# Optimization experiments

Hardware: AMD Instinct MI355X
Metric: run time of the kernel (lower is better)

## Reference

```python
import jax, jax.numpy as jnp
import numpy as np

B, L, D, F = 1, 4096, 4096, 11008
# (start, end, side): side 0 = vision expert, side 1 = language expert.
# Mirrors merge_section_size over alternating contiguous vision/language token ranges.
SEGMENTS = [(0, 1024, 0), (1024, 2048, 1), (2048, 3072, 0), (3072, 4096, 1)]


def setup_inputs() -> dict:
    key = jax.random.key(0)
    ks = jax.random.split(key, 7)
    s = 0.02  # weight init scale
    hidden_states = jax.random.normal(ks[0], (B, L, D), jnp.float32)
    tt = np.zeros((B, L), np.int32)
    for a, b, side in SEGMENTS:
        tt[:, a:b] = side
    token_type_ids = jnp.asarray(tt)
    lg_w = jax.random.normal(ks[1], (D, F), jnp.float32) * s
    lu_w = jax.random.normal(ks[2], (D, F), jnp.float32) * s
    ld_w = jax.random.normal(ks[3], (F, D), jnp.float32) * s
    vg_w = jax.random.normal(ks[4], (D, F), jnp.float32) * s
    vu_w = jax.random.normal(ks[5], (D, F), jnp.float32) * s
    vd_w = jax.random.normal(ks[6], (F, D), jnp.float32) * s
    return {
        'hidden_states': hidden_states,
        'token_type_ids': token_type_ids,
        'lg_w': lg_w, 'lu_w': lu_w, 'ld_w': ld_w,
        'vg_w': vg_w, 'vu_w': vu_w, 'vd_w': vd_w,
    }


def _swiglu_mlp(x, gw, uw, dw):
    # x: [B, T, D] -> [B, T, D]; down(silu(gate(x)) * up(x))
    h = jax.nn.silu(jnp.einsum('btd,df->btf', x, gw)) * jnp.einsum('btd,df->btf', x, uw)
    return jnp.einsum('btf,fd->btd', h, dw)


def reference(hidden_states, token_type_ids, lg_w, lu_w, ld_w, vg_w, vu_w, vd_w):
    # Split-dispatch over static contiguous segments, then concat along seq dim.
    outs = []
    for a, b, side in SEGMENTS:
        seg = hidden_states[:, a:b, :]
        if side == 1:
            outs.append(_swiglu_mlp(seg, lg_w, lu_w, ld_w))
        else:
            outs.append(_swiglu_mlp(seg, vg_w, vu_w, vd_w))
    return jnp.concatenate(outs, axis=1)
```

## Files before the change

### kernel.cpp

```cpp
#include <hip/hip_runtime.h>
#include <math.h>

typedef unsigned short u16;
typedef short s16x8 __attribute__((ext_vector_type(8)));
typedef float f32x4 __attribute__((ext_vector_type(4)));
typedef float f32x16 __attribute__((ext_vector_type(16)));

#define GLOAD16(gp, lp)                                                        \
  __builtin_amdgcn_global_load_lds(                                            \
      (const __attribute__((address_space(1))) void*)(gp),                     \
      (__attribute__((address_space(3))) void*)(lp), 16, 0, 0)

__device__ __forceinline__ u16 f2bf(float f) {
  union { float f; unsigned u; } v; v.f = f;
  unsigned r = v.u + 0x7fffu + ((v.u >> 16) & 1u);
  return (u16)(r >> 16);
}

__global__ __launch_bounds__(256) void cvt_x_kernel(const float* __restrict__ in,
                                                    u16* __restrict__ out) {
  size_t i = ((size_t)blockIdx.x * 256 + threadIdx.x) * 8;
  float4 a = *(const float4*)(in + i);
  float4 b = *(const float4*)(in + i + 4);
  s16x8 v;
  v[0] = (short)f2bf(a.x); v[1] = (short)f2bf(a.y);
  v[2] = (short)f2bf(a.z); v[3] = (short)f2bf(a.w);
  v[4] = (short)f2bf(b.x); v[5] = (short)f2bf(b.y);
  v[6] = (short)f2bf(b.z); v[7] = (short)f2bf(b.w);
  *(s16x8*)(out + i) = v;
}

__global__ __launch_bounds__(256) void transpose_cvt_kernel(
    const float* __restrict__ in0, const float* __restrict__ in1,
    const float* __restrict__ in2, const float* __restrict__ in3,
    const float* __restrict__ in4, const float* __restrict__ in5,
    u16* __restrict__ o01, u16* __restrict__ o23,
    u16* __restrict__ o4, u16* __restrict__ o5) {
  __shared__ float s[64 * 65];
  const int mat = blockIdx.y;
  const float* in; u16* out;
  switch (mat) {
    case 0: in = in0; out = o01; break;
    case 1: in = in1; out = o01; break;
    case 2: in = in2; out = o23; break;
    case 3: in = in3; out = o23; break;
    case 4: in = in4; out = o4; break;
    default: in = in5; out = o5; break;
  }
  const int R = (mat < 4) ? 4096 : 11008;
  const int C = (mat < 4) ? 11008 : 4096;
  const int nTc = C >> 6;
  const int tr = blockIdx.x / nTc, tc = blockIdx.x - tr * nTc;
  const int r0 = tr << 6, c0 = tc << 6;
  const int t = threadIdx.x;
#pragma unroll
  for (int p = 0; p < 4; ++p) {
    const int lr = p * 16 + (t >> 4);
    const int lc = (t & 15) * 4;
    float4 v = *(const float4*)(in + (size_t)(r0 + lr) * C + (c0 + lc));
    float* sp = &s[lr * 65 + lc];
    sp[0] = v.x; sp[1] = v.y; sp[2] = v.z; sp[3] = v.w;
  }
  __syncthreads();
#pragma unroll
  for (int q = 0; q < 2; ++q) {
    const int oc = q * 32 + (t >> 3);
    const int orr = (t & 7) * 8;
    s16x8 v;
#pragma unroll
    for (int i = 0; i < 8; ++i) v[i] = (short)f2bf(s[(orr + i) * 65 + oc]);
    const int f = c0 + oc;
    size_t orow;
    if (mat < 4) orow = (size_t)((f >> 7) << 8) + ((mat & 1) << 7) + (f & 127);
    else         orow = (size_t)f;
    *(s16x8*)(out + orow * R + (r0 + orr)) = v;
  }
}

#define SBAR() __builtin_amdgcn_s_barrier()
#define LGKM0() asm volatile("s_waitcnt lgkmcnt(0)")
#define VMCNT4() asm volatile("s_waitcnt vmcnt(4)")
#define VMCNT2() asm volatile("s_waitcnt vmcnt(2)")
#define VMCNT0() asm volatile("s_waitcnt vmcnt(0)")

#define LDA(d, mh)                                                             \
  do {                                                                         \
    _Pragma("unroll") for (int fj = 0; fj < 2; ++fj)                           \
        _Pragma("unroll") for (int ks = 0; ks < 4; ++ks)                       \
        af[fj][ks] = *(const s16x8*)(ldsA + (d) * 32768 + (mh) * 16384 +       \
                                     arow + fj * 4096 + cx[ks]);               \
  } while (0)
#define LDB(d, nh)                                                             \
  do {                                                                         \
    _Pragma("unroll") for (int ks = 0; ks < 4; ++ks)                           \
        bf[nh][ks] = *(const s16x8*)(ldsB + (d) * 32768 + (nh) * 16384 +       \
                                     brow + cx[ks]);                           \
  } while (0)
#define MFMA8(mh, nh)                                                          \
  do {                                                                         \
    __builtin_amdgcn_s_setprio(1);                                             \
    _Pragma("unroll") for (int fj = 0; fj < 2; ++fj)                           \
        _Pragma("unroll") for (int ks = 0; ks < 4; ++ks)                       \
        acc[mh][fj][nh] = __builtin_amdgcn_mfma_f32_32x32x16_bf16(             \
            af[fj][ks], bf[nh][ks], acc[mh][fj][nh], 0, 0, 0);                 \
    __builtin_amdgcn_s_setprio(0);                                             \
  } while (0)

#define STG_A(d, h, kt)                                                        \
  do {                                                                         \
    GLOAD16(srcA + (size_t)((h) * 128) * KB + (size_t)(kt) * 128,              \
            ldsA + (d) * 32768 + (h) * 16384 + woff);                          \
    GLOAD16(srcA + (size_t)((h) * 128 + 64) * KB + (size_t)(kt) * 128,         \
            ldsA + (d) * 32768 + (h) * 16384 + 8192 + woff);                   \
  } while (0)
#define STG_B(d, h, kt)                                                        \
  do {                                                                         \
    GLOAD16(srcB + (size_t)((h) * 128) * KB + (size_t)(kt) * 128,              \
            ldsB + (d) * 32768 + (h) * 16384 + woff);                          \
    GLOAD16(srcB + (size_t)((h) * 128 + 64) * KB + (size_t)(kt) * 128,         \
            ldsB + (d) * 32768 + (h) * 16384 + 8192 + woff);                   \
  } while (0)

__global__ __launch_bounds__(512, 1) void gemm_gateup_persist(
    const u16* __restrict__ A, const u16* __restrict__ GUl,
    const u16* __restrict__ GUv, const int* __restrict__ tt,
    u16* __restrict__ H, int* __restrict__ qcnt) {
  constexpr int KB = 8192;
  constexpr int NKT = 64;
  __shared__ u16 sA[2][2][128][64];
  __shared__ u16 sB[2][2][128][64];
  __shared__ int sQ;

  const int t = threadIdx.x;
  const int lane = t & 63;
  const int l31 = lane & 31;
  const int kg = lane >> 5;
  const int wn = (t >> 6) & 3;
  const int wm = (t >> 8) & 1;

  const int rowq = t >> 3;
  const int gsw = ((t & 7) ^ (rowq & 7)) << 4;
  char* ldsA = (char*)&sA[0][0][0][0];
  char* ldsB = (char*)&sB[0][0][0][0];
  const int woff = (t & 448) << 4;

  const int arow = (wm * 64 + l31) * 128;
  const int brow = (wn * 32 + l31) * 128;
  int cx[4];
#pragma unroll
  for (int ks = 0; ks < 4; ++ks) cx[ks] = ((2 * ks + kg) ^ (lane & 7)) << 4;

  for (;;) {
    __syncthreads();
    if (t == 0) sQ = atomicAdd(qcnt, 1);
    __syncthreads();
    const int q = sQ;
    if (q >= 1376) break;
    const int nT = q >> 4;
    const int mT = q & 15;
    const int side = tt[mT << 8];
    const u16* GU = side ? GUl : GUv;
    const char* srcA = (const char*)A + (size_t)(mT * 256 + rowq) * KB + gsw;
    const char* srcB = (const char*)GU + (size_t)(nT * 256 + rowq) * KB + gsw;

    s16x8 af[2][4], bf[2][4];
    f32x16 acc[2][2][2];
#pragma unroll
    for (int a = 0; a < 2; ++a)
#pragma unroll
      for (int b = 0; b < 2; ++b)
#pragma unroll
        for (int c = 0; c < 2; ++c)
#pragma unroll
          for (int r = 0; r < 16; ++r) acc[a][b][c][r] = 0.f;

    STG_A(0, 0, 0); STG_B(0, 0, 0); STG_B(0, 1, 0); STG_A(0, 1, 0);
    VMCNT4();
    SBAR();

    for (int T = 0; T < NKT - 1; ++T) {
      const int d = T & 1, nd = d ^ 1;
      LDA(d, 0); LDB(d, 0);
      STG_A(nd, 0, T + 1);
      LGKM0(); MFMA8(0, 0);
      VMCNT4(); SBAR();
      LDB(d, 1);
      STG_B(nd, 0, T + 1);
      LGKM0(); MFMA8(0, 1);
      VMCNT4(); SBAR();
      LDA(d, 1);
      STG_B(nd, 1, T + 1);
      LGKM0(); MFMA8(1, 1);
      STG_A(nd, 1, T + 1);
      MFMA8(1, 0);
      VMCNT4(); SBAR();
    }
    {
      const int d = (NKT - 1) & 1;
      LDA(d, 0); LDB(d, 0);
      LGKM0(); MFMA8(0, 0);
      VMCNT2(); SBAR();
      LDB(d, 1);
      LGKM0(); MFMA8(0, 1);
      VMCNT0(); SBAR();
      LDA(d, 1);
      LGKM0(); MFMA8(1, 1);
      MFMA8(1, 0);
    }

    const int f = nT * 128 + wn * 32 + l31;
#pragma unroll
    for (int mh = 0; mh < 2; ++mh)
#pragma unroll
      for (int fj = 0; fj < 2; ++fj) {
        const int rowbase = mT * 256 + mh * 128 + wm * 64 + fj * 32 + 4 * kg;
#pragma unroll
        for (int r = 0; r < 16; ++r) {
          const int row = rowbase + (r & 3) + 8 * (r >> 2);
          const float gv = acc[mh][fj][0][r];
          const float uv = acc[mh][fj][1][r];
          const float hv = gv / (1.f + __expf(-gv)) * uv;
          H[(size_t)row * 11008 + f] = f2bf(hv);
        }
      }
  }
}

__global__ __launch_bounds__(512, 1) void gemm_down(
    const u16* __restrict__ Hm, const u16* __restrict__ Dl,
    const u16* __restrict__ Dv, const int* __restrict__ tt,
    float* __restrict__ O) {
  constexpr int KB = 22016;
  constexpr int NKT = 172;
  __shared__ u16 sA[2][2][128][64];
  __shared__ u16 sB[2][2][128][64];

  const int bid = blockIdx.x;
  const int wg = (bid & 7) * 32 + (bid >> 3);
  const int mT = wg & 15;
  const int nT = wg >> 4;

  const int t = threadIdx.x;
  const int lane = t & 63;
  const int l31 = lane & 31;
  const int kg = lane >> 5;
  const int wn = (t >> 6) & 3;
  const int wm = (t >> 8) & 1;

  const int side = tt[mT << 8];
  const u16* B = side ? Dl : Dv;

  const int rowq = t >> 3;
  const int gsw = ((t & 7) ^ (rowq & 7)) << 4;
  const char* srcA = (const char*)Hm + (size_t)(mT * 256 + rowq) * KB + gsw;
  const char* srcB = (const char*)B + (size_t)(nT * 256 + rowq) * KB + gsw;
  char* ldsA = (char*)&sA[0][0][0][0];
  char* ldsB = (char*)&sB[0][0][0][0];
  const int woff = (t & 448) << 4;

  const int arow = (wm * 64 + l31) * 128;
  const int brow = (wn * 32 + l31) * 128;
  int cx[4];
#pragma unroll
  for (int ks = 0; ks < 4; ++ks) cx[ks] = ((2 * ks + kg) ^ (lane & 7)) << 4;

  s16x8 af[2][4], bf[2][4];
  f32x16 acc[2][2][2];
#pragma unroll
  for (int a = 0; a < 2; ++a)
#pragma unroll
    for (int b = 0; b < 2; ++b)
#pragma unroll
      for (int c = 0; c < 2; ++c)
#pragma unroll
        for (int r = 0; r < 16; ++r) acc[a][b][c][r] = 0.f;

  STG_A(0, 0, 0); STG_B(0, 0, 0); STG_B(0, 1, 0); STG_A(0, 1, 0);
  VMCNT4();
  SBAR();

  for (int T = 0; T < NKT - 1; ++T) {
    const int d = T & 1, nd = d ^ 1;
    LDA(d, 0); LDB(d, 0);
    STG_A(nd, 0, T + 1);
    LGKM0(); MFMA8(0, 0);
    VMCNT4(); SBAR();
    LDB(d, 1);
    STG_B(nd, 0, T + 1);
    LGKM0(); MFMA8(0, 1);
    VMCNT4(); SBAR();
    LDA(d, 1);
    STG_B(nd, 1, T + 1);
    LGKM0(); MFMA8(1, 1);
    STG_A(nd, 1, T + 1);
    MFMA8(1, 0);
    VMCNT4(); SBAR();
  }
  {
    const int d = (NKT - 1) & 1;
    LDA(d, 0); LDB(d, 0);
    LGKM0(); MFMA8(0, 0);
    VMCNT2(); SBAR();
    LDB(d, 1);
    LGKM0(); MFMA8(0, 1);
    VMCNT0(); SBAR();
    LDA(d, 1);
    LGKM0(); MFMA8(1, 1);
    MFMA8(1, 0);
  }

#pragma unroll
  for (int mh = 0; mh < 2; ++mh)
#pragma unroll
    for (int fj = 0; fj < 2; ++fj) {
      const int rowbase = mT * 256 + mh * 128 + wm * 64 + fj * 32 + 4 * kg;
#pragma unroll
      for (int nh = 0; nh < 2; ++nh) {
        const int col = nT * 256 + nh * 128 + wn * 32 + l31;
#pragma unroll
        for (int r = 0; r < 16; ++r) {
          const int row = rowbase + (r & 3) + 8 * (r >> 2);
          O[(size_t)row * 4096 + col] = acc[mh][fj][nh][r];
        }
      }
    }
}

extern "C" void kernel_launch(void* const* d_in, const int* in_sizes, int n_in,
                              void* d_out, int out_size, void* d_ws, size_t ws_size,
                              hipStream_t stream) {
  (void)in_sizes; (void)n_in; (void)out_size; (void)ws_size;
  const float* x  = (const float*)d_in[0];
  const int*   tt = (const int*)d_in[1];
  const float* lg = (const float*)d_in[2];
  const float* lu = (const float*)d_in[3];
  const float* ld = (const float*)d_in[4];
  const float* vg = (const float*)d_in[5];
  const float* vu = (const float*)d_in[6];
  const float* vd = (const float*)d_in[7];

  u16* ws  = (u16*)d_ws;
  u16* xbf = ws;
  u16* GUl = xbf + 16777216;
  u16* GUv = GUl + 90177536;
  u16* ldT = GUv + 90177536;
  u16* vdT = ldT + 45088768;
  u16* hbuf = vdT + 45088768;
  int* qcnt = (int*)(hbuf + 45088768);

  hipMemsetAsync(qcnt, 0, 4, stream);
  cvt_x_kernel<<<dim3(8192), dim3(256), 0, stream>>>(x, xbf);
  transpose_cvt_kernel<<<dim3(11008, 6), dim3(256), 0, stream>>>(
      lg, lu, vg, vu, ld, vd, GUl, GUv, ldT, vdT);
  gemm_gateup_persist<<<dim3(256), dim3(512), 0, stream>>>(
      xbf, GUl, GUv, tt, hbuf, qcnt);
  gemm_down<<<dim3(256), dim3(512), 0, stream>>>(hbuf, ldT, vdT, tt, (float*)d_out);
}
```

Baseline: 1.410 ms.

## Restructure GEMM main loop into 8-wave ping-pong pipeline with deeper prefetch

Replaces the per-k-tile main loop in both GEMMs with a shared macro that unrolls two k-tiles, issues loads for up to two tiles ahead, and wraps each MFMA cluster in barriers so wave groups alternate between loading and computing. Wait counts change to allow more global loads in flight. The LDS swizzle also gains an extra XOR term on row bits 3-4 to reduce bank conflicts on fragment reads. The extra barriers add synchronisation overhead, and the new prefetch order and wait counts must stay correct for the buffer reuse.

```diff
diff --git a/kernel.cpp b/kernel.cpp
--- a/kernel.cpp
+++ b/kernel.cpp
@@ -3,7 +3,6 @@
 
 typedef unsigned short u16;
 typedef short s16x8 __attribute__((ext_vector_type(8)));
-typedef float f32x4 __attribute__((ext_vector_type(4)));
 typedef float f32x16 __attribute__((ext_vector_type(16)));
 
 #define GLOAD16(gp, lp)                                                        \
@@ -79,8 +78,8 @@
 
 #define SBAR() __builtin_amdgcn_s_barrier()
 #define LGKM0() asm volatile("s_waitcnt lgkmcnt(0)")
-#define VMCNT4() asm volatile("s_waitcnt vmcnt(4)")
-#define VMCNT2() asm volatile("s_waitcnt vmcnt(2)")
+#define LGKM8() asm volatile("s_waitcnt lgkmcnt(8)")
+#define VMCNT6() asm volatile("s_waitcnt vmcnt(6)")
 #define VMCNT0() asm volatile("s_waitcnt vmcnt(0)")
 
 #define LDA(d, mh)                                                             \
@@ -121,12 +120,65 @@
             ldsB + (d) * 32768 + (h) * 16384 + 8192 + woff);                   \
   } while (0)
 
+#define GEMM_PIPE(NKT)                                                         \
+  do {                                                                         \
+    STG_A(0, 0, 0); STG_B(0, 0, 0); STG_B(0, 1, 0); STG_A(0, 1, 0);            \
+    STG_A(1, 0, 1); STG_B(1, 0, 1); STG_B(1, 1, 1);                            \
+    VMCNT6();                                                                  \
+    SBAR();                                                                    \
+    for (int T = 0; T < (NKT)-2; T += 2) {                                     \
+      LDA(0, 0); LDB(0, 0);                                                    \
+      STG_A(1, 1, T + 1);                                                      \
+      LGKM8();                                                                 \
+      SBAR(); LGKM0(); MFMA8(0, 0); SBAR();                                    \
+      LDB(0, 1);                                                               \
+      STG_A(0, 0, T + 2);                                                      \
+      SBAR(); LGKM0(); MFMA8(0, 1); SBAR();                                    \
+      LDA(0, 1);                                                               \
+      STG_B(0, 0, T + 2);                                                      \
+      SBAR(); LGKM0(); MFMA8(1, 1); SBAR();                                    \
+      STG_B(0, 1, T + 2);                                                      \
+      VMCNT6();                                                                \
+      SBAR(); MFMA8(1, 0); SBAR();                                             \
+      LDA(1, 0); LDB(1, 0);                                                    \
+      STG_A(0, 1, T + 2);                                                      \
+      LGKM8();                                                                 \
+      SBAR(); LGKM0(); MFMA8(0, 0); SBAR();                                    \
+      LDB(1, 1);                                                               \
+      STG_A(1, 0, T + 3);                                                      \
+      SBAR(); LGKM0(); MFMA8(0, 1); SBAR();                                    \
+      LDA(1, 1);                                                               \
+      STG_B(1, 0, T + 3);                                                      \
+      SBAR(); LGKM0(); MFMA8(1, 1); SBAR();                                    \
+      STG_B(1, 1, T + 3);                                                      \
+      VMCNT6();                                                                \
+      SBAR(); MFMA8(1, 0); SBAR();                                             \
+    }                                                                          \
+    LDA(0, 0); LDB(0, 0);                                                      \
+    STG_A(1, 1, (NKT)-1);                                                      \
+    LGKM8();                                                                   \
+    SBAR(); LGKM0(); MFMA8(0, 0); SBAR();                                      \
+    LDB(0, 1);                                                                 \
+    SBAR(); LGKM0(); MFMA8(0, 1); SBAR();                                      \
+    LDA(0, 1);                                                                 \
+    SBAR(); LGKM0(); MFMA8(1, 1); SBAR();                                      \
+    VMCNT0();                                                                  \
+    SBAR(); MFMA8(1, 0); SBAR();                                               \
+    LDA(1, 0); LDB(1, 0);                                                      \
+    LGKM8();                                                                   \
+    SBAR(); LGKM0(); MFMA8(0, 0); SBAR();                                      \
+    LDB(1, 1);                                                                 \
+    SBAR(); LGKM0(); MFMA8(0, 1); SBAR();                                      \
+    LDA(1, 1);                                                                 \
+    SBAR(); LGKM0(); MFMA8(1, 1); SBAR();                                      \
+    MFMA8(1, 0);                                                               \
+  } while (0)
+
 __global__ __launch_bounds__(512, 1) void gemm_gateup_persist(
     const u16* __restrict__ A, const u16* __restrict__ GUl,
     const u16* __restrict__ GUv, const int* __restrict__ tt,
     u16* __restrict__ H, int* __restrict__ qcnt) {
   constexpr int KB = 8192;
-  constexpr int NKT = 64;
   __shared__ u16 sA[2][2][128][64];
   __shared__ u16 sB[2][2][128][64];
   __shared__ int sQ;
@@ -139,7 +191,7 @@
   const int wm = (t >> 8) & 1;
 
   const int rowq = t >> 3;
-  const int gsw = ((t & 7) ^ (rowq & 7)) << 4;
+  const int gsw = ((t & 7) ^ (rowq & 7) ^ ((rowq >> 3) & 3)) << 4;
   char* ldsA = (char*)&sA[0][0][0][0];
   char* ldsB = (char*)&sB[0][0][0][0];
   const int woff = (t & 448) << 4;
@@ -148,7 +200,8 @@
   const int brow = (wn * 32 + l31) * 128;
   int cx[4];
 #pragma unroll
-  for (int ks = 0; ks < 4; ++ks) cx[ks] = ((2 * ks + kg) ^ (lane & 7)) << 4;
+  for (int ks = 0; ks < 4; ++ks)
+    cx[ks] = ((2 * ks + kg) ^ (l31 & 7) ^ ((l31 >> 3) & 3)) << 4;
 
   for (;;) {
     __syncthreads();
@@ -170,43 +223,11 @@
 #pragma unroll
       for (int b = 0; b < 2; ++b)
 #pragma unroll
-        for (int c = 0; c < 2; ++c)
-#pragma unroll
-          for (int r = 0; r < 16; ++r) acc[a][b][c][r] = 0.f;
-
-    STG_A(0, 0, 0); STG_B(0, 0, 0); STG_B(0, 1, 0); STG_A(0, 1, 0);
-    VMCNT4();
-    SBAR();
-
-    for (int T = 0; T < NKT - 1; ++T) {
-      const int d = T & 1, nd = d ^ 1;
-      LDA(d, 0); LDB(d, 0);
-      STG_A(nd, 0, T + 1);
-      LGKM0(); MFMA8(0, 0);
-      VMCNT4(); SBAR();
-      LDB(d, 1);
-      STG_B(nd, 0, T + 1);
-      LGKM0(); MFMA8(0, 1);
-      VMCNT4(); SBAR();
-      LDA(d, 1);
-      STG_B(nd, 1, T + 1);
-      LGKM0(); MFMA8(1, 1);
-      STG_A(nd, 1, T + 1);
-      MFMA8(1, 0);
-      VMCNT4(); SBAR();
-    }
-    {
-      const int d = (NKT - 1) & 1;
-      LDA(d, 0); LDB(d, 0);
-      LGKM0(); MFMA8(0, 0);
-      VMCNT2(); SBAR();
-      LDB(d, 1);
-      LGKM0(); MFMA8(0, 1);
-      VMCNT0(); SBAR();
-      LDA(d, 1);
-      LGKM0(); MFMA8(1, 1);
-      MFMA8(1, 0);
-    }
+        for (int c2 = 0; c2 < 2; ++c2)
+#pragma unroll
+          for (int r = 0; r < 16; ++r) acc[a][b][c2][r] = 0.f;
+
+    GEMM_PIPE(64);
 
     const int f = nT * 128 + wn * 32 + l31;
 #pragma unroll
@@ -231,7 +252,6 @@
     const u16* __restrict__ Dv, const int* __restrict__ tt,
     float* __restrict__ O) {
   constexpr int KB = 22016;
-  constexpr int NKT = 172;
   __shared__ u16 sA[2][2][128][64];
   __shared__ u16 sB[2][2][128][64];
 
@@ -251,7 +271,7 @@
   const u16* B = side ? Dl : Dv;
 
   const int rowq = t >> 3;
-  const int gsw = ((t & 7) ^ (rowq & 7)) << 4;
+  const int gsw = ((t & 7) ^ (rowq & 7) ^ ((rowq >> 3) & 3)) << 4;
   const char* srcA = (const char*)Hm + (size_t)(mT * 256 + rowq) * KB + gsw;
   const char* srcB = (const char*)B + (size_t)(nT * 256 + rowq) * KB + gsw;
   char* ldsA = (char*)&sA[0][0][0][0];
@@ -262,7 +282,8 @@
   const int brow = (wn * 32 + l31) * 128;
   int cx[4];
 #pragma unroll
-  for (int ks = 0; ks < 4; ++ks) cx[ks] = ((2 * ks + kg) ^ (lane & 7)) << 4;
+  for (int ks = 0; ks < 4; ++ks)
+    cx[ks] = ((2 * ks + kg) ^ (l31 & 7) ^ ((l31 >> 3) & 3)) << 4;
 
   s16x8 af[2][4], bf[2][4];
   f32x16 acc[2][2][2];
@@ -271,43 +292,11 @@
 #pragma unroll
     for (int b = 0; b < 2; ++b)
 #pragma unroll
-      for (int c = 0; c < 2; ++c)
-#pragma unroll
-        for (int r = 0; r < 16; ++r) acc[a][b][c][r] = 0.f;
-
-  STG_A(0, 0, 0); STG_B(0, 0, 0); STG_B(0, 1, 0); STG_A(0, 1, 0);
-  VMCNT4();
-  SBAR();
-
-  for (int T = 0; T < NKT - 1; ++T) {
-    const int d = T & 1, nd = d ^ 1;
-    LDA(d, 0); LDB(d, 0);
-    STG_A(nd, 0, T + 1);
-    LGKM0(); MFMA8(0, 0);
-    VMCNT4(); SBAR();
-    LDB(d, 1);
-    STG_B(nd, 0, T + 1);
-    LGKM0(); MFMA8(0, 1);
-    VMCNT4(); SBAR();
-    LDA(d, 1);
-    STG_B(nd, 1, T + 1);
-    LGKM0(); MFMA8(1, 1);
-    STG_A(nd, 1, T + 1);
-    MFMA8(1, 0);
-    VMCNT4(); SBAR();
-  }
-  {
-    const int d = (NKT - 1) & 1;
-    LDA(d, 0); LDB(d, 0);
-    LGKM0(); MFMA8(0, 0);
-    VMCNT2(); SBAR();
-    LDB(d, 1);
-    LGKM0(); MFMA8(0, 1);
-    VMCNT0(); SBAR();
-    LDA(d, 1);
-    LGKM0(); MFMA8(1, 1);
-    MFMA8(1, 0);
-  }
+      for (int c2 = 0; c2 < 2; ++c2)
+#pragma unroll
+        for (int r = 0; r < 16; ++r) acc[a][b][c2][r] = 0.f;
+
+  GEMM_PIPE(172);
 
 #pragma unroll
   for (int mh = 0; mh < 2; ++mh)
```

Measured after the change: 1.362 ms. -3.4%, faster.
